# Performance work log

Hardware: AMD Instinct MI355X
Metric: run time of the kernel (lower is better)

## Reference

```python
import jax, jax.numpy as jnp
import numpy as np

NEG_SLOPE = 0.2
EPS = 1e-16


def gat_layer(x, src, dst, W, att, bias, heads, out_ch, concat, num_nodes, edge_weight):
    """WeightedGATConv forward (eval mode, dropout off).
    x: [N, Fin], src/dst: [E], W: [Fin, H*C], att: [H, 2C], bias: [H*C] or [C].
    """
    H, C = heads, out_ch
    xp = (x @ W).reshape(-1, H, C)           # [N, H, C]
    xi = xp[dst]                              # target features  [E, H, C]
    xj = xp[src]                              # source features  [E, H, C]
    # attention logits: (cat(xi, xj) * att).sum(-1)
    alpha = jnp.einsum('ehc,hc->eh', xi, att[:, :C]) + jnp.einsum('ehc,hc->eh', xj, att[:, C:])
    alpha = jnp.where(alpha >= 0, alpha, NEG_SLOPE * alpha)   # leaky_relu
    # segment softmax over incoming edges of each destination node
    amax = jax.ops.segment_max(alpha, dst, num_segments=num_nodes)  # [N, H]
    amax = jnp.where(jnp.isfinite(amax), amax, 0.0)
    ex = jnp.exp(alpha - amax[dst])                                  # [E, H]
    denom = jax.ops.segment_sum(ex, dst, num_segments=num_nodes)     # [N, H]
    a = ex / (denom[dst] + EPS)                                      # [E, H]
    msg = xj * a[..., None]                                          # [E, H, C]
    if edge_weight is not None:
        msg = msg * edge_weight[:, None, None]
    out = jax.ops.segment_sum(msg, dst, num_segments=num_nodes)      # [N, H, C]
    out = out.reshape(num_nodes, H * C) if concat else out.mean(axis=1)
    return out + bias


def setup_inputs() -> dict:
    key = jax.random.key(0)
    ks = jax.random.split(key, 10)
    N, E = 20000, 320000
    IN, HID, LAT, H = 512, 256, 128, 4
    C1 = HID // H
    glorot = lambda k, shp: jax.random.uniform(k, shp, jnp.float32, -1.0, 1.0) * jnp.sqrt(6.0 / (shp[-2] + shp[-1]))
    return {
        'x': jax.random.normal(ks[0], (N, IN), jnp.float32),
        'edge_index': jax.random.randint(ks[1], (2, E), 0, N, jnp.int32),
        'edge_weight': jax.random.uniform(ks[2], (E,), jnp.float32),
        'W1': glorot(ks[3], (IN, H * C1)),
        'att1': glorot(ks[4], (H, 2 * C1)),
        'b1': jnp.zeros((H * C1,), jnp.float32),
        'Wmu': glorot(ks[5], (HID, LAT)),
        'attmu': glorot(ks[6], (1, 2 * LAT)),
        'bmu': jnp.zeros((LAT,), jnp.float32),
        'Wlv': glorot(ks[7], (HID, LAT)),
        'attlv': glorot(ks[8], (1, 2 * LAT)),
        'blv': jnp.zeros((LAT,), jnp.float32),
    }


def reference(x, edge_index, edge_weight, W1, att1, b1, Wmu, attmu, bmu, Wlv, attlv, blv):
    N = x.shape[0]
    src, dst = edge_index[0], edge_index[1]
    H = att1.shape[0]
    C1 = att1.shape[1] // 2
    LAT = Wmu.shape[1]
    h = gat_layer(x, src, dst, W1, att1, b1, H, C1, True, N, edge_weight)
    h = jax.nn.elu(h)
    mu = gat_layer(h, src, dst, Wmu, attmu, bmu, 1, LAT, False, N, edge_weight)
    logvar = gat_layer(h, src, dst, Wlv, attlv, blv, 1, LAT, False, N, edge_weight)
    return (mu, logvar)
```

## Files before the change

### kernel.cpp

```cpp
#include <hip/hip_runtime.h>
#include <stdint.h>

#define NEG_SLOPE 0.2f
#define SEPS 1e-16f

typedef short bf16x8 __attribute__((ext_vector_type(8)));
typedef float f32x4 __attribute__((ext_vector_type(4)));

static __device__ __forceinline__ float bf2f(ushort u) {
  union { uint32_t i; float f; } v; v.i = ((uint32_t)u) << 16; return v.f;
}
static __device__ __forceinline__ ushort f2bf(float f) {
  uint32_t b = __float_as_uint(f);
  b += 0x7FFFu + ((b >> 16) & 1u);
  return (ushort)(b >> 16);
}
static __device__ __forceinline__ float blo(uint32_t u) { return __uint_as_float(u << 16); }
static __device__ __forceinline__ float bhi(uint32_t u) { return __uint_as_float(u & 0xFFFF0000u); }
static __device__ __forceinline__ float ldf(const void* p, size_t i, int mode) {
  return mode ? ((const float*)p)[i] : bf2f(((const ushort*)p)[i]);
}

__global__ void fill_out(float* __restrict__ out, int n, float v) {
  int i = blockIdx.x * 256 + threadIdx.x;
  if (i < n) out[i] = v;
}

struct DetPtrs {
  const uint32_t* p[11];
  int n[11];
  const uint32_t* idx;
  int idxn;
};
__global__ void prologue(DetPtrs dp, int* __restrict__ modes,
                         int* __restrict__ deg, int N) {
  int b = blockIdx.x;
  if (b >= 12) {
    int i = (b - 12) * 256 + threadIdx.x;
    if (i < N) deg[i] = 0;
    return;
  }
  __shared__ int sL, sH;
  if (threadIdx.x == 0) { sL = 0; sH = 0; }
  __syncthreads();
  if (b < 11) {
    const uint32_t* w = dp.p[b];
    int elems = dp.n[b];
    int nprobe = min(2048, elems / 2);
    int cL = 0, cH = 0;
    for (int i = threadIdx.x; i < nprobe; i += 256) {
      uint32_t v = w[i];
      uint32_t eL = (v >> 7) & 0xFFu;
      uint32_t eH = (v >> 23) & 0xFFu;
      if (eL >= 90u && eL <= 128u) cL++;
      if (eH >= 90u && eH <= 128u) cH++;
    }
    atomicAdd(&sL, cL); atomicAdd(&sH, cH);
    __syncthreads();
    if (threadIdx.x == 0) {
      int m;
      if (sL * 4 >= nprobe * 3) m = 0;
      else if (sH * 4 >= nprobe) m = 1;
      else m = 0;
      modes[b] = m;
    }
  } else {
    const uint32_t* w = dp.idx;
    int nprobe = min(4096, dp.idxn);
    int c = 0;
    for (int i = threadIdx.x; i < nprobe; i += 256)
      if ((i & 1) && w[i] == 0u) c++;
    atomicAdd(&sL, c);
    __syncthreads();
    if (threadIdx.x == 0) modes[11] = (sL * 4 >= (nprobe / 2) * 3) ? 1 : 0;
  }
}

struct WTArgs {
  const void* w1; const void* wmu; const void* wlv;
  ushort* wt1; ushort* wall;
};
struct SmallCan { const void* src[6]; float* dst[6]; int n[6]; int mi[6]; };
struct CanArgs {
  const void* ei; const void* ew;
  int* srcc; int* dstc; int* deg; float* ewf;
  int E; int N; int EB1; int WB;
  WTArgs wt;
  SmallCan sc;
};
__global__ void canon_all(CanArgs a, const int* __restrict__ modes) {
  int b = blockIdx.x;
  if (b < a.EB1) {
    int i = b * 256 + threadIdx.x;
    if (i >= a.E) return;
    int s, d;
    if (modes[11]) {
      s = (int)((const long long*)a.ei)[i];
      d = (int)((const long long*)a.ei)[a.E + i];
    } else {
      s = ((const int*)a.ei)[i];
      d = ((const int*)a.ei)[a.E + i];
    }
    s = min(max(s, 0), a.N - 1);
    d = min(max(d, 0), a.N - 1);
    a.srcc[i] = s;
    a.dstc[i] = d;
    atomicAdd(&a.deg[d], 1);
    float v = ldf(a.ew, i, modes[1]);
    if (!isfinite(v)) v = 0.f;
    a.ewf[i] = v;
  } else if (b < a.EB1 + a.WB) {
    int i = (b - a.EB1) * 256 + threadIdx.x;
    const int NW1 = 256 * 512;
    if (i < NW1) {
      int n = i >> 9, k = i & 511;
      float v = ldf(a.wt.w1, (size_t)k * 256 + n, modes[2]);
      if (!isfinite(v)) v = 0.f;
      a.wt.wt1[i] = f2bf(v);
    } else {
      int j = i - NW1;
      if (j >= 256 * 256) return;
      int n = j >> 8, k = j & 255;
      float v;
      if (n < 128) v = ldf(a.wt.wmu, (size_t)k * 128 + n, modes[5]);
      else         v = ldf(a.wt.wlv, (size_t)k * 128 + (n - 128), modes[8]);
      if (!isfinite(v)) v = 0.f;
      a.wt.wall[j] = f2bf(v);
    }
  } else {
    int sb = b - a.EB1 - a.WB;
    int m = modes[a.sc.mi[sb]];
    const void* s = a.sc.src[sb];
    float* d = a.sc.dst[sb];
    for (int i = threadIdx.x; i < a.sc.n[sb]; i += 256) {
      float v = ldf(s, i, m);
      if (!isfinite(v)) v = 0.f;
      d[i] = v;
    }
  }
}

__global__ __launch_bounds__(1024) void scan_deg(const int* __restrict__ deg,
                                                 int* __restrict__ row_ptr,
                                                 int* __restrict__ row_cur, int N) {
  __shared__ int part[1024];
  int t = threadIdx.x;
  int chunk = (N + 1023) / 1024;
  int lo = t * chunk, hi = min(lo + chunk, N);
  int s = 0;
  for (int i = lo; i < hi; ++i) s += deg[i];
  part[t] = s;
  __syncthreads();
  for (int off = 1; off < 1024; off <<= 1) {
    int v = (t >= off) ? part[t - off] : 0;
    __syncthreads();
    part[t] += v;
    __syncthreads();
  }
  int base = (t == 0) ? 0 : part[t - 1];
  for (int i = lo; i < hi; ++i) {
    row_ptr[i] = base; row_cur[i] = base;
    base += deg[i];
  }
  if (t == 1023) row_ptr[N] = part[1023];
}
__global__ void scatter_edges(const int* __restrict__ dstv, const int* __restrict__ srcv,
                              const float* __restrict__ ew, int* __restrict__ row_cur,
                              int* __restrict__ csr_src, float* __restrict__ csr_w, int E) {
  int e = blockIdx.x * 256 + threadIdx.x;
  if (e < E) {
    int p = atomicAdd(&row_cur[dstv[e]], 1);
    csr_src[p] = srcv[e];
    csr_w[p] = ew[e];
  }
}

template <int KTOT, int DMODE>
__global__ __launch_bounds__(256) void gemm_mfma(
    const void* __restrict__ A, const ushort* __restrict__ WT,
    ushort* __restrict__ out, int M,
    const int* __restrict__ modeA, const float* __restrict__ attv,
    float* __restrict__ dotd, float* __restrict__ dotsrc) {
  __shared__ ushort As[64][40];
  __shared__ ushort Bs[256][40];

  int t = threadIdx.x;
  int m0 = blockIdx.x * 64;
  int wid = t >> 6, l = t & 63;
  int wr = wid >> 1, wc = wid & 1;
  int mode = modeA ? *modeA : 0;

  int arow = t >> 2;
  int akoff = (t & 3) * 8;
  int srow = min(m0 + arow, M - 1);

  f32x4 acc[2][8];
#pragma unroll
  for (int i = 0; i < 2; ++i)
#pragma unroll
    for (int j = 0; j < 8; ++j) acc[i][j] = (f32x4){0.f, 0.f, 0.f, 0.f};

  int cl = l & 15;
  int ksl = (l >> 4) * 8;

  for (int k0 = 0; k0 < KTOT; k0 += 32) {
    if (mode) {
      const float* Af = (const float*)A + (size_t)srow * KTOT + k0 + akoff;
      float4 v0 = *(const float4*)Af;
      float4 v1 = *(const float4*)(Af + 4);
      uint4 pk;
      pk.x = (uint32_t)f2bf(v0.x) | ((uint32_t)f2bf(v0.y) << 16);
      pk.y = (uint32_t)f2bf(v0.z) | ((uint32_t)f2bf(v0.w) << 16);
      pk.z = (uint32_t)f2bf(v1.x) | ((uint32_t)f2bf(v1.y) << 16);
      pk.w = (uint32_t)f2bf(v1.z) | ((uint32_t)f2bf(v1.w) << 16);
      *(uint4*)&As[arow][akoff] = pk;
    } else {
      *(uint4*)&As[arow][akoff] =
          *(const uint4*)((const ushort*)A + (size_t)srow * KTOT + k0 + akoff);
    }
#pragma unroll
    for (int i = 0; i < 4; ++i) {
      int f = t + i * 256;
      int row = f >> 2, koff = (f & 3) * 8;
      *(uint4*)&Bs[row][koff] = *(const uint4*)(WT + (size_t)row * KTOT + k0 + koff);
    }
    __syncthreads();

    bf16x8 af[2], bfr[8];
#pragma unroll
    for (int i = 0; i < 2; ++i)
      af[i] = *(const bf16x8*)&As[wr * 32 + i * 16 + cl][ksl];
#pragma unroll
    for (int j = 0; j < 8; ++j)
      bfr[j] = *(const bf16x8*)&Bs[wc * 128 + j * 16 + cl][ksl];
#pragma unroll
    for (int i = 0; i < 2; ++i)
#pragma unroll
      for (int j = 0; j < 8; ++j)
        acc[i][j] = __builtin_amdgcn_mfma_f32_16x16x32_bf16(af[i], bfr[j], acc[i][j], 0, 0, 0);
    __syncthreads();
  }

  int rb = (l >> 4) * 4;

  if (DMODE == 1) {
    float wdv[8], wsv[8];
#pragma unroll
    for (int j = 0; j < 8; ++j) {
      int h = wc * 2 + (j >> 2);
      int c = (j & 3) * 16 + cl;
      wdv[j] = attv[h * 128 + c];
      wsv[j] = attv[h * 128 + 64 + c];
    }
#pragma unroll
    for (int i = 0; i < 2; ++i)
#pragma unroll
      for (int r = 0; r < 4; ++r) {
        float pd0 = acc[i][0][r] * wdv[0] + acc[i][1][r] * wdv[1]
                  + acc[i][2][r] * wdv[2] + acc[i][3][r] * wdv[3];
        float ps0 = acc[i][0][r] * wsv[0] + acc[i][1][r] * wsv[1]
                  + acc[i][2][r] * wsv[2] + acc[i][3][r] * wsv[3];
        float pd1 = acc[i][4][r] * wdv[4] + acc[i][5][r] * wdv[5]
                  + acc[i][6][r] * wdv[6] + acc[i][7][r] * wdv[7];
        float ps1 = acc[i][4][r] * wsv[4] + acc[i][5][r] * wsv[5]
                  + acc[i][6][r] * wsv[6] + acc[i][7][r] * wsv[7];
#pragma unroll
        for (int d = 1; d < 16; d <<= 1) {
          pd0 += __shfl_xor(pd0, d); ps0 += __shfl_xor(ps0, d);
          pd1 += __shfl_xor(pd1, d); ps1 += __shfl_xor(ps1, d);
        }
        if (cl == 0) {
          int m = m0 + wr * 32 + i * 16 + rb + r;
          if (m < M) {
            dotd[m * 4 + wc * 2] = pd0;
            dotsrc[m * 4 + wc * 2] = ps0;
            dotd[m * 4 + wc * 2 + 1] = pd1;
            dotsrc[m * 4 + wc * 2 + 1] = ps1;
          }
        }
      }
  } else if (DMODE == 2) {
    float wdv[8], wsv[8];
#pragma unroll
    for (int j = 0; j < 8; ++j) {
      int c = j * 16 + cl;
      wdv[j] = attv[wc * 256 + c];
      wsv[j] = attv[wc * 256 + 128 + c];
    }
#pragma unroll
    for (int i = 0; i < 2; ++i)
#pragma unroll
      for (int r = 0; r < 4; ++r) {
        float pd = 0.f, ps = 0.f;
#pragma unroll
        for (int j = 0; j < 8; ++j) {
          pd += acc[i][j][r] * wdv[j];
          ps += acc[i][j][r] * wsv[j];
        }
#pragma unroll
        for (int d = 1; d < 16; d <<= 1) {
          pd += __shfl_xor(pd, d); ps += __shfl_xor(ps, d);
        }
        if (cl == 0) {
          int m = m0 + wr * 32 + i * 16 + rb + r;
          if (m < M) {
            dotd[m * 4 + wc * 2] = pd;
            dotd[m * 4 + wc * 2 + 1] = ps;
          }
        }
      }
  }

#pragma unroll
  for (int i = 0; i < 2; ++i)
#pragma unroll
    for (int j = 0; j < 8; ++j)
#pragma unroll
      for (int r = 0; r < 4; ++r) {
        int m = m0 + wr * 32 + i * 16 + rb + r;
        if (m < M)
          out[(size_t)m * 256 + wc * 128 + j * 16 + cl] = f2bf(acc[i][j][r]);
      }
}

__global__ __launch_bounds__(256) void fused_agg1_wave(
    const int* __restrict__ row_ptr, const int* __restrict__ csr_src,
    const float* __restrict__ csr_w,
    const float* __restrict__ ad, const float* __restrict__ as_,
    const ushort* __restrict__ xp, const float* __restrict__ b1,
    ushort* __restrict__ hout, int N) {
  int n = blockIdx.x * 4 + (threadIdx.x >> 6);
  if (n >= N) return;
  int lane = threadIdx.x & 63;
  int h = lane & 3;
  int es = lane >> 2;
  int sg = lane >> 5, l = lane & 31, hl = l >> 3;

  int lo = row_ptr[n], hi = row_ptr[n + 1];
  float adv = ad[n * 4 + h];

  float m = -1e30f;
  float dsum = 0.f;
  float acc[8];
#pragma unroll
  for (int j = 0; j < 8; ++j) acc[j] = 0.f;

  for (int cb = lo; cb < hi; cb += 16) {
    int cn = min(16, hi - cb);
    float a = -1e30f;
    int sreg = 0;
    float wreg = 0.f;
    if (es < cn) {
      int i = cb + es;
      int s = csr_src[i];
      sreg = s;
      wreg = csr_w[i];
      float aa = adv + as_[s * 4 + h];
      a = aa >= 0.f ? aa : NEG_SLOPE * aa;
    }
    float cm = a;
    cm = fmaxf(cm, __shfl_xor(cm, 4));
    cm = fmaxf(cm, __shfl_xor(cm, 8));
    cm = fmaxf(cm, __shfl_xor(cm, 16));
    cm = fmaxf(cm, __shfl_xor(cm, 32));
    float mnew = fmaxf(m, cm);
    float scale = expf(m - mnew);
    m = mnew;
    float ev = (es < cn) ? expf(a - m) : 0.f;
    dsum = dsum * scale + ev;
    float cwreg = ev * wreg;
    float sc = __shfl(scale, hl);
#pragma unroll
    for (int j = 0; j < 8; ++j) acc[j] *= sc;
    for (int el2 = 0; el2 < cn; el2 += 2) {
      int el = el2 + sg;
      int elc = min(el, cn - 1);
      float cw = __shfl(cwreg, (elc << 2) | hl);
      int s = __shfl(sreg, elc << 2);
      if (el < cn) {
        uint4 v = *(const uint4*)(xp + (size_t)s * 256 + l * 8);
        acc[0] += cw * blo(v.x); acc[1] += cw * bhi(v.x);
        acc[2] += cw * blo(v.y); acc[3] += cw * bhi(v.y);
        acc[4] += cw * blo(v.z); acc[5] += cw * bhi(v.z);
        acc[6] += cw * blo(v.w); acc[7] += cw * bhi(v.w);
      }
    }
  }

  dsum += __shfl_xor(dsum, 4);
  dsum += __shfl_xor(dsum, 8);
  dsum += __shfl_xor(dsum, 16);
  dsum += __shfl_xor(dsum, 32);
  float den = __shfl(dsum, hl);

#pragma unroll
  for (int j = 0; j < 8; ++j) acc[j] += __shfl_down(acc[j], 32);

  if (sg == 0) {
    float inv = 1.0f / (den + SEPS);
    uint4 pk;
    uint32_t w[4];
#pragma unroll
    for (int q = 0; q < 4; ++q) {
      float v0 = acc[q * 2] * inv + b1[l * 8 + q * 2];
      float v1 = acc[q * 2 + 1] * inv + b1[l * 8 + q * 2 + 1];
      v0 = v0 > 0.f ? v0 : expm1f(v0);
      v1 = v1 > 0.f ? v1 : expm1f(v1);
      w[q] = (uint32_t)f2bf(v0) | ((uint32_t)f2bf(v1) << 16);
    }
    pk.x = w[0]; pk.y = w[1]; pk.z = w[2]; pk.w = w[3];
    *(uint4*)(hout + (size_t)n * 256 + l * 8) = pk;
  }
}

__global__ __launch_bounds__(256) void fused_agg2_wave(
    const int* __restrict__ row_ptr, const int* __restrict__ csr_src,
    const float* __restrict__ csr_w, const float* __restrict__ a4,
    const ushort* __restrict__ hp2,
    const float* __restrict__ bmu, const float* __restrict__ blv,
    float* __restrict__ out, int N) {
  int n = blockIdx.x * 4 + (threadIdx.x >> 6);
  if (n >= N) return;
  int lane = threadIdx.x & 63;
  int e31 = lane & 31, sl = lane >> 5;

  int lo = row_ptr[n], hi = row_ptr[n + 1];
  float adv = a4[n * 4 + sl * 2];

  float m = -1e30f;
  float dsum = 0.f;
  float acc[4];
#pragma unroll
  for (int j = 0; j < 4; ++j) acc[j] = 0.f;

  for (int cb = lo; cb < hi; cb += 32) {
    int cn = min(32, hi - cb);
    float a = -1e30f;
    int sreg = 0;
    float wreg = 0.f;
    if (e31 < cn) {
      int i = cb + e31;
      int s = csr_src[i];
      sreg = s;
      wreg = csr_w[i];
      float aa = adv + a4[s * 4 + sl * 2 + 1];
      a = aa >= 0.f ? aa : NEG_SLOPE * aa;
    }
    float cm = a;
    cm = fmaxf(cm, __shfl_xor(cm, 1));
    cm = fmaxf(cm, __shfl_xor(cm, 2));
    cm = fmaxf(cm, __shfl_xor(cm, 4));
    cm = fmaxf(cm, __shfl_xor(cm, 8));
    cm = fmaxf(cm, __shfl_xor(cm, 16));
    float mnew = fmaxf(m, cm);
    float scale = expf(m - mnew);
    m = mnew;
    float ev = (e31 < cn) ? expf(a - m) : 0.f;
    dsum = dsum * scale + ev;
    float cwreg = ev * wreg;
#pragma unroll
    for (int j = 0; j < 4; ++j) acc[j] *= scale;
    for (int el = 0; el < cn; ++el) {
      float cw = __shfl(cwreg, (sl << 5) | el);
      int s = __shfl(sreg, el);
      uint2 v = *(const uint2*)(hp2 + (size_t)s * 256 + lane * 4);
      acc[0] += cw * blo(v.x); acc[1] += cw * bhi(v.x);
      acc[2] += cw * blo(v.y); acc[3] += cw * bhi(v.y);
    }
  }

  dsum += __shfl_xor(dsum, 1);
  dsum += __shfl_xor(dsum, 2);
  dsum += __shfl_xor(dsum, 4);
  dsum += __shfl_xor(dsum, 8);
  dsum += __shfl_xor(dsum, 16);

  float inv = 1.0f / (dsum + SEPS);
  const float* bb = sl ? blv : bmu;
  int c0 = e31 * 4;
  float* op = out + (size_t)sl * N * 128 + (size_t)n * 128 + c0;
#pragma unroll
  for (int j = 0; j < 4; ++j) op[j] = acc[j] * inv + bb[c0 + j];
}

extern "C" void kernel_launch(void* const* d_in, const int* in_sizes, int n_in,
                              void* d_out, int out_size, void* d_ws, size_t ws_size,
                              hipStream_t stream) {
  int OB = (out_size + 255) / 256;
  bool ok = (n_in == 12);
  int HID = 0, IN = 0, N = 0, LAT = 0, E = 0;
  if (ok) {
    HID = in_sizes[5];
    ok = ok && HID == 256;
    IN = HID ? in_sizes[3] / HID : 0;
    ok = ok && IN == 512 && in_sizes[3] == IN * HID;
    N = IN ? in_sizes[0] / IN : 0;
    ok = ok && N > 0 && in_sizes[0] == N * IN && (N % 4) == 0;
    LAT = in_sizes[8];
    ok = ok && LAT == 128;
    E = in_sizes[2];
    ok = ok && E > 0 && in_sizes[1] == 2 * E;
    ok = ok && in_sizes[4] == 2 * HID && in_sizes[6] == HID * LAT &&
         in_sizes[7] == 2 * LAT && in_sizes[9] == HID * LAT &&
         in_sizes[10] == 2 * LAT && in_sizes[11] == LAT &&
         out_size == 2 * N * LAT;
  }
  if (!ok) { fill_out<<<OB, 256, 0, stream>>>((float*)d_out, out_size, 2.0f); return; }

  char* p = (char*)d_ws;
  auto alloc = [&](size_t bytes) -> char* {
    char* r = p;
    p += (bytes + 255) & ~((size_t)255);
    return r;
  };
  ushort* xp_bf = (ushort*)alloc((size_t)N * HID * 2);
  ushort* hreg  = (ushort*)alloc((size_t)N * HID * 2);
  ushort* WT1b  = (ushort*)alloc((size_t)HID * IN * 2);
  ushort* WallT = (ushort*)alloc((size_t)2 * LAT * HID * 2);
  float*  dots  = (float*) alloc((size_t)N * 12 * 4);
  float*  att1f = (float*) alloc((size_t)2 * HID * 4);
  float*  att2f = (float*) alloc((size_t)4 * LAT * 4);
  float*  b1f   = (float*) alloc((size_t)HID * 4);
  float*  bmuf  = (float*) alloc((size_t)LAT * 4);
  float*  blvf  = (float*) alloc((size_t)LAT * 4);
  float*  ewf   = (float*) alloc((size_t)E * 4);
  int*    srcc  = (int*)   alloc((size_t)E * 4);
  int*    dstc  = (int*)   alloc((size_t)E * 4);
  int*    csr_src=(int*)   alloc((size_t)E * 4);
  float*  csr_w = (float*) alloc((size_t)E * 4);
  int*    row_ptr=(int*)   alloc((size_t)(N + 1) * 4);
  int*    row_cur=(int*)   alloc((size_t)N * 4);
  int*    deg   = (int*)   alloc((size_t)N * 4);
  int*    modes = (int*)   alloc(16 * 4);

  size_t need = (size_t)(p - (char*)d_ws);
  if (need > ws_size) {
    fill_out<<<OB, 256, 0, stream>>>((float*)d_out, out_size, 3.0f);
    return;
  }

  ushort* hp2 = xp_bf;
  float* ad1 = dots;
  float* as1 = dots + (size_t)N * 4;
  float* a4  = dots + (size_t)N * 8;

  const int fidx[11] = {0, 2, 3, 4, 5, 6, 7, 8, 9, 10, 11};
  DetPtrs dp;
  for (int i = 0; i < 11; ++i) {
    dp.p[i] = (const uint32_t*)d_in[fidx[i]];
    dp.n[i] = in_sizes[fidx[i]];
  }
  dp.idx = (const uint32_t*)d_in[1];
  dp.idxn = 2 * E;
  int nbDeg = (N + 255) / 256;
  prologue<<<12 + nbDeg, 256, 0, stream>>>(dp, modes, deg, N);

  int EB1 = (E + 255) / 256;
  int WB = (HID * IN + 2 * LAT * HID + 255) / 256;
  CanArgs ca;
  ca.ei = d_in[1]; ca.ew = d_in[2];
  ca.srcc = srcc; ca.dstc = dstc; ca.deg = deg; ca.ewf = ewf;
  ca.E = E; ca.N = N; ca.EB1 = EB1; ca.WB = WB;
  ca.wt.w1 = d_in[3]; ca.wt.wmu = d_in[6]; ca.wt.wlv = d_in[9];
  ca.wt.wt1 = WT1b; ca.wt.wall = WallT;
  ca.sc.src[0] = d_in[4];  ca.sc.dst[0] = att1f;        ca.sc.n[0] = 2 * HID; ca.sc.mi[0] = 3;
  ca.sc.src[1] = d_in[5];  ca.sc.dst[1] = b1f;          ca.sc.n[1] = HID;     ca.sc.mi[1] = 4;
  ca.sc.src[2] = d_in[7];  ca.sc.dst[2] = att2f;        ca.sc.n[2] = 2 * LAT; ca.sc.mi[2] = 6;
  ca.sc.src[3] = d_in[8];  ca.sc.dst[3] = bmuf;         ca.sc.n[3] = LAT;     ca.sc.mi[3] = 7;
  ca.sc.src[4] = d_in[10]; ca.sc.dst[4] = att2f + 256;  ca.sc.n[4] = 2 * LAT; ca.sc.mi[4] = 9;
  ca.sc.src[5] = d_in[11]; ca.sc.dst[5] = blvf;         ca.sc.n[5] = LAT;     ca.sc.mi[5] = 10;
  canon_all<<<EB1 + WB + 6, 256, 0, stream>>>(ca, modes);

  scan_deg<<<1, 1024, 0, stream>>>(deg, row_ptr, row_cur, N);
  scatter_edges<<<EB1, 256, 0, stream>>>(dstc, srcc, ewf, row_cur, csr_src, csr_w, E);

  int MB = (N + 63) / 64;

  gemm_mfma<512, 1><<<MB, 256, 0, stream>>>(d_in[0], WT1b, xp_bf, N,
                                            &modes[0], att1f, ad1, as1);
  fused_agg1_wave<<<(N + 3) / 4, 256, 0, stream>>>(row_ptr, csr_src, csr_w,
                                                   ad1, as1, xp_bf, b1f, hreg, N);

  gemm_mfma<256, 2><<<MB, 256, 0, stream>>>(hreg, WallT, hp2, N,
                                            nullptr, att2f, a4, nullptr);
  fused_agg2_wave<<<(N + 3) / 4, 256, 0, stream>>>(row_ptr, csr_src, csr_w, a4,
                                                   hp2, bmuf, blvf,
                                                   (float*)d_out, N);
}
```

Baseline: 286.3 us.

## Fuse edge scatter into GEMM launch and widen aggregation gather loads

The CSR edge-scatter kernel is folded into the first GEMM launch as extra leading blocks, which removes one kernel launch and lets the scatter overlap with the GEMM. The layer-1 aggregation loop is unrolled to issue two independent 16-byte gathers per iteration, adding memory-level parallelism. The layer-2 aggregation is restructured to use 16-byte loads, with half-waves processing alternate edges and a cross-half reduction at the end, in place of narrow per-edge 8-byte loads. Running scatter blocks next to GEMM blocks may compete for resources, and the extra live registers may lower occupancy.

```diff
diff --git a/kernel.cpp b/kernel.cpp
--- a/kernel.cpp
+++ b/kernel.cpp
@@ -164,28 +164,31 @@
   }
   if (t == 1023) row_ptr[N] = part[1023];
 }
-__global__ void scatter_edges(const int* __restrict__ dstv, const int* __restrict__ srcv,
-                              const float* __restrict__ ew, int* __restrict__ row_cur,
-                              int* __restrict__ csr_src, float* __restrict__ csr_w, int E) {
-  int e = blockIdx.x * 256 + threadIdx.x;
-  if (e < E) {
-    int p = atomicAdd(&row_cur[dstv[e]], 1);
-    csr_src[p] = srcv[e];
-    csr_w[p] = ew[e];
-  }
-}
 
 template <int KTOT, int DMODE>
-__global__ __launch_bounds__(256) void gemm_mfma(
+__global__ __launch_bounds__(256) void gemm_mfma_sc(
     const void* __restrict__ A, const ushort* __restrict__ WT,
     ushort* __restrict__ out, int M,
     const int* __restrict__ modeA, const float* __restrict__ attv,
-    float* __restrict__ dotd, float* __restrict__ dotsrc) {
+    float* __restrict__ dotd, float* __restrict__ dotsrc,
+    int SB, const int* __restrict__ dstv, const int* __restrict__ srcv,
+    const float* __restrict__ ew, int* __restrict__ row_cur,
+    int* __restrict__ csr_src, float* __restrict__ csr_w, int E) {
   __shared__ ushort As[64][40];
   __shared__ ushort Bs[256][40];
 
+  if ((int)blockIdx.x < SB) {
+    int e = blockIdx.x * 256 + threadIdx.x;
+    if (e < E) {
+      int p = atomicAdd(&row_cur[dstv[e]], 1);
+      csr_src[p] = srcv[e];
+      csr_w[p] = ew[e];
+    }
+    return;
+  }
+
   int t = threadIdx.x;
-  int m0 = blockIdx.x * 64;
+  int m0 = (blockIdx.x - SB) * 64;
   int wid = t >> 6, l = t & 63;
   int wr = wid >> 1, wc = wid & 1;
   int mode = modeA ? *modeA : 0;
@@ -372,17 +375,28 @@
     float sc = __shfl(scale, hl);
 #pragma unroll
     for (int j = 0; j < 8; ++j) acc[j] *= sc;
-    for (int el2 = 0; el2 < cn; el2 += 2) {
-      int el = el2 + sg;
-      int elc = min(el, cn - 1);
-      float cw = __shfl(cwreg, (elc << 2) | hl);
-      int s = __shfl(sreg, elc << 2);
-      if (el < cn) {
-        uint4 v = *(const uint4*)(xp + (size_t)s * 256 + l * 8);
-        acc[0] += cw * blo(v.x); acc[1] += cw * bhi(v.x);
-        acc[2] += cw * blo(v.y); acc[3] += cw * bhi(v.y);
-        acc[4] += cw * blo(v.z); acc[5] += cw * bhi(v.z);
-        acc[6] += cw * blo(v.w); acc[7] += cw * bhi(v.w);
+    for (int el2 = 0; el2 < cn; el2 += 4) {
+      int ea = el2 + sg, eb = el2 + 2 + sg;
+      int eac = min(ea, cn - 1), ebc = min(eb, cn - 1);
+      float cwa = __shfl(cwreg, (eac << 2) | hl);
+      int sa = __shfl(sreg, eac << 2);
+      float cwb = __shfl(cwreg, (ebc << 2) | hl);
+      int sb = __shfl(sreg, ebc << 2);
+      bool pa = ea < cn, pb = eb < cn;
+      uint4 va, vb;
+      if (pa) va = *(const uint4*)(xp + (size_t)sa * 256 + l * 8);
+      if (pb) vb = *(const uint4*)(xp + (size_t)sb * 256 + l * 8);
+      if (pa) {
+        acc[0] += cwa * blo(va.x); acc[1] += cwa * bhi(va.x);
+        acc[2] += cwa * blo(va.y); acc[3] += cwa * bhi(va.y);
+        acc[4] += cwa * blo(va.z); acc[5] += cwa * bhi(va.z);
+        acc[6] += cwa * blo(va.w); acc[7] += cwa * bhi(va.w);
+      }
+      if (pb) {
+        acc[0] += cwb * blo(vb.x); acc[1] += cwb * bhi(vb.x);
+        acc[2] += cwb * blo(vb.y); acc[3] += cwb * bhi(vb.y);
+        acc[4] += cwb * blo(vb.z); acc[5] += cwb * bhi(vb.z);
+        acc[6] += cwb * blo(vb.w); acc[7] += cwb * bhi(vb.w);
       }
     }
   }
@@ -422,16 +436,21 @@
   int n = blockIdx.x * 4 + (threadIdx.x >> 6);
   if (n >= N) return;
   int lane = threadIdx.x & 63;
-  int e31 = lane & 31, sl = lane >> 5;
+  int e31 = lane & 31;
+  int half = lane >> 5;
+  int sg = lane >> 5;
+  int l = lane & 31;
+  int hh = l >> 4;
+  int hlane = hh << 5;
 
   int lo = row_ptr[n], hi = row_ptr[n + 1];
-  float adv = a4[n * 4 + sl * 2];
+  float adv = a4[n * 4 + half * 2];
 
   float m = -1e30f;
   float dsum = 0.f;
-  float acc[4];
-#pragma unroll
-  for (int j = 0; j < 4; ++j) acc[j] = 0.f;
+  float acc[8];
+#pragma unroll
+  for (int j = 0; j < 8; ++j) acc[j] = 0.f;
 
   for (int cb = lo; cb < hi; cb += 32) {
     int cn = min(32, hi - cb);
@@ -443,7 +462,7 @@
       int s = csr_src[i];
       sreg = s;
       wreg = csr_w[i];
-      float aa = adv + a4[s * 4 + sl * 2 + 1];
+      float aa = adv + a4[s * 4 + half * 2 + 1];
       a = aa >= 0.f ? aa : NEG_SLOPE * aa;
     }
     float cm = a;
@@ -458,14 +477,21 @@
     float ev = (e31 < cn) ? expf(a - m) : 0.f;
     dsum = dsum * scale + ev;
     float cwreg = ev * wreg;
-#pragma unroll
-    for (int j = 0; j < 4; ++j) acc[j] *= scale;
-    for (int el = 0; el < cn; ++el) {
-      float cw = __shfl(cwreg, (sl << 5) | el);
-      int s = __shfl(sreg, el);
-      uint2 v = *(const uint2*)(hp2 + (size_t)s * 256 + lane * 4);
-      acc[0] += cw * blo(v.x); acc[1] += cw * bhi(v.x);
-      acc[2] += cw * blo(v.y); acc[3] += cw * bhi(v.y);
+    float sc = __shfl(scale, hlane);
+#pragma unroll
+    for (int j = 0; j < 8; ++j) acc[j] *= sc;
+    for (int el2 = 0; el2 < cn; el2 += 2) {
+      int el = el2 + sg;
+      int elc = min(el, cn - 1);
+      float cw = __shfl(cwreg, elc | (hh << 5));
+      int s = __shfl(sreg, elc);
+      if (el < cn) {
+        uint4 v = *(const uint4*)(hp2 + (size_t)s * 256 + l * 8);
+        acc[0] += cw * blo(v.x); acc[1] += cw * bhi(v.x);
+        acc[2] += cw * blo(v.y); acc[3] += cw * bhi(v.y);
+        acc[4] += cw * blo(v.z); acc[5] += cw * bhi(v.z);
+        acc[6] += cw * blo(v.w); acc[7] += cw * bhi(v.w);
+      }
     }
   }
 
@@ -474,13 +500,19 @@
   dsum += __shfl_xor(dsum, 4);
   dsum += __shfl_xor(dsum, 8);
   dsum += __shfl_xor(dsum, 16);
-
-  float inv = 1.0f / (dsum + SEPS);
-  const float* bb = sl ? blv : bmu;
-  int c0 = e31 * 4;
-  float* op = out + (size_t)sl * N * 128 + (size_t)n * 128 + c0;
-#pragma unroll
-  for (int j = 0; j < 4; ++j) op[j] = acc[j] * inv + bb[c0 + j];
+  float den = __shfl(dsum, hlane);
+
+#pragma unroll
+  for (int j = 0; j < 8; ++j) acc[j] += __shfl_down(acc[j], 32);
+
+  if (sg == 0) {
+    float inv = 1.0f / (den + SEPS);
+    const float* bb = hh ? blv : bmu;
+    int c0 = (l & 15) * 8;
+    float* op = out + (size_t)hh * N * 128 + (size_t)n * 128 + c0;
+#pragma unroll
+    for (int j = 0; j < 8; ++j) op[j] = acc[j] * inv + bb[c0 + j];
+  }
 }
 
 extern "C" void kernel_launch(void* const* d_in, const int* in_sizes, int n_in,
@@ -572,17 +604,18 @@
   canon_all<<<EB1 + WB + 6, 256, 0, stream>>>(ca, modes);
 
   scan_deg<<<1, 1024, 0, stream>>>(deg, row_ptr, row_cur, N);
-  scatter_edges<<<EB1, 256, 0, stream>>>(dstc, srcc, ewf, row_cur, csr_src, csr_w, E);
 
   int MB = (N + 63) / 64;
 
-  gemm_mfma<512, 1><<<MB, 256, 0, stream>>>(d_in[0], WT1b, xp_bf, N,
-                                            &modes[0], att1f, ad1, as1);
+  gemm_mfma_sc<512, 1><<<EB1 + MB, 256, 0, stream>>>(
+      d_in[0], WT1b, xp_bf, N, &modes[0], att1f, ad1, as1,
+      EB1, dstc, srcc, ewf, row_cur, csr_src, csr_w, E);
   fused_agg1_wave<<<(N + 3) / 4, 256, 0, stream>>>(row_ptr, csr_src, csr_w,
                                                    ad1, as1, xp_bf, b1f, hreg, N);
 
-  gemm_mfma<256, 2><<<MB, 256, 0, stream>>>(hreg, WallT, hp2, N,
-                                            nullptr, att2f, a4, nullptr);
+  gemm_mfma_sc<256, 2><<<MB, 256, 0, stream>>>(
+      hreg, WallT, hp2, N, nullptr, att2f, a4, nullptr,
+      0, nullptr, nullptr, nullptr, nullptr, nullptr, nullptr, 0);
   fused_agg2_wave<<<(N + 3) / 4, 256, 0, stream>>>(row_ptr, csr_src, csr_w, a4,
                                                    hp2, bmuf, blvf,
                                                    (float*)d_out, N);
```

Result: faster. 280.4 us (-2.1%).
